# Optimization experiments

Hardware: AMD Instinct MI355X
Metric: run time of the kernel (lower is better)

Reference implementation:

```python
import jax, jax.numpy as jnp
import numpy as np

B, S, D = 4, 1024, 384
NUM_ITEMS = 16384
NUM_CLUSTERS = 256
MAX_CLUSTER_SIZE = 128  # 16384/256 = 64 real members, padded to 128 with -1
NEG_INF = -1e9


def setup_inputs() -> dict:
    key = jax.random.key(0)
    k1, k2, k3, k4, k5 = jax.random.split(key, 5)
    hidden_states = jax.random.normal(k1, (B, S, D), dtype=jnp.float32)
    item_embeddings = jax.random.normal(k2, (NUM_ITEMS, D), dtype=jnp.float32) * 0.02
    cluster_embeddings = jax.random.normal(k3, (NUM_CLUSTERS, D), dtype=jnp.float32) * 0.02
    targets = jax.random.randint(k4, (B, S), 0, NUM_ITEMS, dtype=jnp.int32)
    item_mask = (jax.random.uniform(k5, (B, S)) < 0.8).astype(jnp.float32)
    # Deterministic round-robin clustering: item i -> cluster i % C, slot i // C
    cluster_assignments = (jnp.arange(NUM_ITEMS, dtype=jnp.int32) % NUM_CLUSTERS)
    ids = (jnp.arange(NUM_CLUSTERS, dtype=jnp.int32)[:, None]
           + NUM_CLUSTERS * jnp.arange(MAX_CLUSTER_SIZE, dtype=jnp.int32)[None, :])
    cluster_indices = jnp.where(ids < NUM_ITEMS, ids, -1)  # [C, M], padded with -1
    in_cluster_id = (jnp.arange(NUM_ITEMS, dtype=jnp.int32) // NUM_CLUSTERS)
    return {
        "hidden_states": hidden_states,
        "item_embeddings": item_embeddings,
        "cluster_embeddings": cluster_embeddings,
        "item_mask": item_mask,
        "targets": targets,
        "cluster_assignments": cluster_assignments,
        "cluster_indices": cluster_indices,
        "in_cluster_id": in_cluster_id,
    }


def reference(hidden_states, item_embeddings, cluster_embeddings, item_mask,
              targets, cluster_assignments, cluster_indices, in_cluster_id):
    # Level 1: cluster logits / log-probs
    cluster_logits = jnp.einsum('bsd,cd->bsc', hidden_states, cluster_embeddings)
    cluster_log_probs = jax.nn.log_softmax(cluster_logits, axis=-1)
    target_cluster_ids = cluster_assignments[targets]                      # [B,S]
    target_cluster_log_prob = jnp.take_along_axis(
        cluster_log_probs, target_cluster_ids[..., None].astype(jnp.int32), axis=-1
    ).squeeze(-1)                                                          # [B,S]

    # Level 2: gather member embeddings of the target cluster, masked softmax
    cluster_members = cluster_indices[target_cluster_ids]                  # [B,S,M]
    member_emb = item_embeddings[jnp.maximum(cluster_members, 0)]          # [B,S,M,D]
    member_logits = jnp.einsum('bsd,bsmd->bsm', hidden_states, member_emb)  # [B,S,M]
    masked_logits = jnp.where(cluster_members != -1, member_logits, NEG_INF)
    member_log_probs = jax.nn.log_softmax(masked_logits, axis=-1)
    target_pos = in_cluster_id[targets]                                    # [B,S]
    target_item_log_prob = jnp.take_along_axis(
        member_log_probs, target_pos[..., None].astype(jnp.int32), axis=-1
    ).squeeze(-1)

    # Combined loss
    loss_per_token = -(target_cluster_log_prob + target_item_log_prob)
    total_loss = jnp.sum(loss_per_token * item_mask) / (jnp.sum(item_mask) + 1e-8)

    cluster_preds = jnp.argmax(cluster_logits, axis=-1)
    cluster_acc = jnp.mean((cluster_preds == target_cluster_ids).astype(jnp.float32))

    dummy_logits = jnp.zeros(hidden_states.shape[:2] + (item_embeddings.shape[0],),
                             dtype=hidden_states.dtype)
    return (dummy_logits, total_loss,
            -jnp.mean(target_cluster_log_prob),
            -jnp.mean(target_item_log_prob),
            cluster_acc)
```

## Files before the change

kernel.cpp:

```cpp
#include <hip/hip_runtime.h>
#include <math.h>

#define Ddim 384
#define D4 96
#define NUM_ITEMS 16384
#define NUM_CLUSTERS 256
#define MCS 128
#define NEG_INF_F (-1e9f)
#define NTOK 4096
#define TPB 8
#define NCB (NTOK / TPB)
#define NFILLB 2048

__device__ __forceinline__ float dot4(const float4& a, const float4& b) {
    return a.x * b.x + a.y * b.y + a.z * b.z + a.w * b.w;
}

__global__ __launch_bounds__(256) void hs_fill_meta(
    const int* __restrict__ targets, const int* __restrict__ cluster_assign,
    float* __restrict__ dummy_out, int* __restrict__ wsI)
{
    const int tid = threadIdx.x;

    if (blockIdx.x == NFILLB) {
        __shared__ int cnt[NUM_CLUSTERS], scan[NUM_CLUSTERS], cur[NUM_CLUSTERS];
        cnt[tid] = 0; cur[tid] = 0;
        __syncthreads();
        int tcv[NTOK / 256];
        #pragma unroll
        for (int i = 0; i < NTOK / 256; ++i) {
            const int t = i * 256 + tid;
            const int tc = cluster_assign[targets[t]];
            tcv[i] = tc;
            atomicAdd(&cnt[tc], 1);
        }
        __syncthreads();
        scan[tid] = cnt[tid];
        __syncthreads();
        for (int d = 1; d < 256; d <<= 1) {
            const int v = (tid >= d) ? scan[tid - d] : 0;
            __syncthreads();
            scan[tid] += v;
            __syncthreads();
        }
        wsI[tid] = scan[tid] - cnt[tid];
        if (tid == 255) wsI[256] = NTOK;
        __syncthreads();
        #pragma unroll
        for (int i = 0; i < NTOK / 256; ++i) {
            const int t = i * 256 + tid;
            const int tc = tcv[i];
            const int p = atomicAdd(&cur[tc], 1);
            wsI[257 + (scan[tc] - cnt[tc]) + p] = t;
        }
        return;
    }

    const size_t base = (size_t)blockIdx.x * 256 + tid;
    float4 z; z.x = z.y = z.z = z.w = 0.f;
    float4* o4 = reinterpret_cast<float4*>(dummy_out) + base;
    #pragma unroll 8
    for (int i = 0; i < 32; ++i)
        o4[(size_t)i * (NFILLB * 256)] = z;
}

__global__ __launch_bounds__(512, 2) void hs_compute(
    const float* __restrict__ hidden,
    const float* __restrict__ item_emb,
    const float* __restrict__ cluster_emb,
    const float* __restrict__ item_mask,
    const int*   __restrict__ targets,
    const int*   __restrict__ cluster_assign,
    const int*   __restrict__ cluster_idx,
    const int*   __restrict__ in_cluster_id,
    const int*   __restrict__ wsI,
    float* __restrict__ ws)
{
    const int cb   = blockIdx.x;
    const int tid  = threadIdx.x;
    const int t0   = cb * TPB;
    const int lane = tid & 63;
    const int wave = tid >> 6;
    const int wq   = wave & 1;
    const int wqt  = wave >> 1;
    const int q    = lane >> 4;
    const int r    = lane & 15;

    __shared__ float clog[TPB][NUM_CLUSTERS];
    __shared__ float mlog[TPB][64];

    const int* list = wsI + 257;

    const float4* h4 = reinterpret_cast<const float4*>(hidden);
    int tok[4];
    #pragma unroll
    for (int j = 0; j < 4; ++j) tok[j] = list[t0 + wq * 4 + j];
    float4 hf[4][6];
    #pragma unroll
    for (int j = 0; j < 4; ++j)
        #pragma unroll
        for (int i = 0; i < 6; ++i)
            hf[j][i] = h4[(size_t)tok[j] * D4 + i * 16 + r];

    const float4* ce4 = reinterpret_cast<const float4*>(cluster_emb);
    #pragma unroll 2
    for (int it = 0; it < 16; ++it) {
        const int c = wqt * 64 + it * 4 + q;
        float4 ce[6];
        #pragma unroll
        for (int i = 0; i < 6; ++i) ce[i] = ce4[(size_t)c * D4 + i * 16 + r];
        float a0 = 0.f, a1 = 0.f, a2 = 0.f, a3 = 0.f;
        #pragma unroll
        for (int i = 0; i < 6; ++i) {
            a0 += dot4(ce[i], hf[0][i]);
            a1 += dot4(ce[i], hf[1][i]);
            a2 += dot4(ce[i], hf[2][i]);
            a3 += dot4(ce[i], hf[3][i]);
        }
        const bool hi8 = (r & 8) != 0;
        float u  = hi8 ? a1 : a0;
        float uS = hi8 ? a0 : a1;
        u += __shfl_xor(uS, 8);
        float w  = hi8 ? a3 : a2;
        float wS = hi8 ? a2 : a3;
        w += __shfl_xor(wS, 8);
        const bool hi4 = (r & 4) != 0;
        float zv = hi4 ? w : u;
        float zS = hi4 ? u : w;
        zv += __shfl_xor(zS, 4);
        zv += __shfl_xor(zv, 2);
        zv += __shfl_xor(zv, 1);
        if ((r & 3) == 0) {
            const int m = (r >> 2) & 3;
            const int tokj = (m == 1) ? 2 : (m == 2) ? 1 : m;
            clog[wq * 4 + tokj][c] = zv;
        }
    }
    __syncthreads();

    const int r8 = lane & 7;
    const int g8 = lane >> 3;
    const float4* ie4 = reinterpret_cast<const float4*>(item_emb);

    const int t  = wave;
    const int gt = list[t0 + t];
    const int tgt  = targets[gt];
    const int tc   = cluster_assign[tgt];
    const int tpos = in_cluster_id[tgt];
    const float msk = item_mask[gt];

    const float v0 = clog[t][lane];
    const float v1 = clog[t][lane + 64];
    const float v2 = clog[t][lane + 128];
    const float v3 = clog[t][lane + 192];
    float bv = v0; int bi = lane;
    if (v1 > bv) { bv = v1; bi = lane + 64;  }
    if (v2 > bv) { bv = v2; bi = lane + 128; }
    if (v3 > bv) { bv = v3; bi = lane + 192; }
    #pragma unroll
    for (int m = 32; m > 0; m >>= 1) {
        const float ov = __shfl_xor(bv, m);
        const int   oi = __shfl_xor(bi, m);
        if (ov > bv || (ov == bv && oi < bi)) { bv = ov; bi = oi; }
    }
    float e = expf(v0 - bv) + expf(v1 - bv) + expf(v2 - bv) + expf(v3 - bv);
    #pragma unroll
    for (int m = 32; m > 0; m >>= 1) e += __shfl_xor(e, m);
    const float lse = bv + logf(e);
    const float tlpc = clog[t][tc] - lse;

    float4 hme[12];
    #pragma unroll
    for (int i = 0; i < 12; ++i)
        hme[i] = h4[(size_t)gt * D4 + i * 8 + r8];
    const int* crow = cluster_idx + (size_t)tc * MCS;
    #pragma unroll 2
    for (int it = 0; it < 8; ++it) {
        const int id = crow[it * 8 + g8];
        const float4* ir = ie4 + (size_t)id * D4;
        float pa = 0.f;
        #pragma unroll
        for (int i = 0; i < 12; ++i) pa += dot4(ir[i * 8 + r8], hme[i]);
        pa += __shfl_xor(pa, 1);
        pa += __shfl_xor(pa, 2);
        pa += __shfl_xor(pa, 4);
        if (r8 == 0) mlog[t][it * 8 + g8] = pa;
    }
    const float w0 = mlog[t][lane];
    float mx = w0;
    #pragma unroll
    for (int m = 32; m > 0; m >>= 1) mx = fmaxf(mx, __shfl_xor(mx, m));
    float e2 = expf(w0 - mx);
    #pragma unroll
    for (int m = 32; m > 0; m >>= 1) e2 += __shfl_xor(e2, m);
    const float tlpi = mlog[t][tpos] - (mx + logf(e2));

    if (lane == 0) {
        ws[NTOK + gt]     = msk;
        ws[2 * NTOK + gt] = tlpc;
        ws[3 * NTOK + gt] = tlpi;
        ws[4 * NTOK + gt] = (bi == tc) ? 1.f : 0.f;
    }
}

__global__ __launch_bounds__(1024) void hs_final(
    const float* __restrict__ ws, float* __restrict__ out)
{
    __shared__ double red[5][1024];
    const int tid = threadIdx.x;
    double a0 = 0, a1 = 0, a2 = 0, a3 = 0, a4 = 0;
    for (int i = tid; i < NTOK; i += 1024) {
        const float msk  = ws[NTOK + i];
        const float tlpc = ws[2 * NTOK + i];
        const float tlpi = ws[3 * NTOK + i];
        a0 += (double)(-(tlpc + tlpi) * msk);
        a1 += (double)msk;
        a2 += (double)tlpc;
        a3 += (double)tlpi;
        a4 += (double)ws[4 * NTOK + i];
    }
    red[0][tid] = a0; red[1][tid] = a1; red[2][tid] = a2;
    red[3][tid] = a3; red[4][tid] = a4;
    __syncthreads();
    for (int s2 = 512; s2 > 0; s2 >>= 1) {
        if (tid < s2) {
            red[0][tid] += red[0][tid + s2];
            red[1][tid] += red[1][tid + s2];
            red[2][tid] += red[2][tid + s2];
            red[3][tid] += red[3][tid + s2];
            red[4][tid] += red[4][tid + s2];
        }
        __syncthreads();
    }
    if (tid == 0) {
        out[0] = (float)(red[0][0] / (red[1][0] + 1e-8));
        out[1] = (float)(-red[2][0] / (double)NTOK);
        out[2] = (float)(-red[3][0] / (double)NTOK);
        out[3] = (float)(red[4][0] / (double)NTOK);
    }
}

extern "C" void kernel_launch(void* const* d_in, const int* in_sizes, int n_in,
                              void* d_out, int out_size, void* d_ws, size_t ws_size,
                              hipStream_t stream) {
    const float* hidden         = (const float*)d_in[0];
    const float* item_emb       = (const float*)d_in[1];
    const float* cluster_emb    = (const float*)d_in[2];
    const float* item_mask      = (const float*)d_in[3];
    const int*   targets        = (const int*)d_in[4];
    const int*   cluster_assign = (const int*)d_in[5];
    const int*   cluster_idx    = (const int*)d_in[6];
    const int*   in_cluster_id  = (const int*)d_in[7];

    float* out = (float*)d_out;
    float* ws  = (float*)d_ws;
    int*   wsI = (int*)(ws + 5 * NTOK);

    const size_t dummy_elems = (size_t)NTOK * NUM_ITEMS;

    hs_fill_meta<<<NFILLB + 1, 256, 0, stream>>>(
        targets, cluster_assign, out, wsI);
    hs_compute<<<NCB, 512, 0, stream>>>(
        hidden, item_emb, cluster_emb, item_mask, targets,
        cluster_assign, cluster_idx, in_cluster_id, wsI, ws);
    hs_final<<<1, 1024, 0, stream>>>(ws, out + dummy_elems);
}
```

Measured before the change: 108.2 us.

## Use 256-thread blocks with each wave scoring all eight tokens per cluster

The compute kernel drops to 4 waves per block. Each wave now holds hidden-state fragments for all 8 tokens and scores 64 clusters against them, so every cluster row is loaded once per block instead of twice. The shuffle reduction is reworked to a 5-bit lane split, and an empty asm pins the hidden registers. Each wave then runs the member-softmax phase for 2 tokens in turn, which reduces parallelism in that phase and raises register pressure.

```diff
diff --git a/kernel.cpp b/kernel.cpp
--- a/kernel.cpp
+++ b/kernel.cpp
@@ -15,6 +15,9 @@
 __device__ __forceinline__ float dot4(const float4& a, const float4& b) {
     return a.x * b.x + a.y * b.y + a.z * b.z + a.w * b.w;
 }
+__device__ __forceinline__ void pin4(float4& v) {
+    asm volatile("" : "+v"(v.x), "+v"(v.y), "+v"(v.z), "+v"(v.w));
+}
 
 __global__ __launch_bounds__(256) void hs_fill_meta(
     const int* __restrict__ targets, const int* __restrict__ cluster_assign,
@@ -64,7 +67,7 @@
         o4[(size_t)i * (NFILLB * 256)] = z;
 }
 
-__global__ __launch_bounds__(512, 2) void hs_compute(
+__global__ __launch_bounds__(256, 2) void hs_compute(
     const float* __restrict__ hidden,
     const float* __restrict__ item_emb,
     const float* __restrict__ cluster_emb,
@@ -81,10 +84,8 @@
     const int t0   = cb * TPB;
     const int lane = tid & 63;
     const int wave = tid >> 6;
-    const int wq   = wave & 1;
-    const int wqt  = wave >> 1;
-    const int q    = lane >> 4;
-    const int r    = lane & 15;
+    const int q2   = lane >> 5;
+    const int r5   = lane & 31;
 
     __shared__ float clog[TPB][NUM_CLUSTERS];
     __shared__ float mlog[TPB][64];
@@ -92,48 +93,60 @@
     const int* list = wsI + 257;
 
     const float4* h4 = reinterpret_cast<const float4*>(hidden);
-    int tok[4];
+    int tok[8];
     #pragma unroll
-    for (int j = 0; j < 4; ++j) tok[j] = list[t0 + wq * 4 + j];
-    float4 hf[4][6];
+    for (int j = 0; j < 8; ++j) tok[j] = list[t0 + j];
+    float4 hf[8][3];
     #pragma unroll
-    for (int j = 0; j < 4; ++j)
-        #pragma unroll
-        for (int i = 0; i < 6; ++i)
-            hf[j][i] = h4[(size_t)tok[j] * D4 + i * 16 + r];
+    for (int j = 0; j < 8; ++j)
+        #pragma unroll
+        for (int i = 0; i < 3; ++i) {
+            hf[j][i] = h4[(size_t)tok[j] * D4 + i * 32 + r5];
+            pin4(hf[j][i]);
+        }
 
     const float4* ce4 = reinterpret_cast<const float4*>(cluster_emb);
     #pragma unroll 2
-    for (int it = 0; it < 16; ++it) {
-        const int c = wqt * 64 + it * 4 + q;
-        float4 ce[6];
-        #pragma unroll
-        for (int i = 0; i < 6; ++i) ce[i] = ce4[(size_t)c * D4 + i * 16 + r];
+    for (int it = 0; it < 32; ++it) {
+        const int c = wave * 64 + it * 2 + q2;
+        float4 ce[3];
+        #pragma unroll
+        for (int i = 0; i < 3; ++i) ce[i] = ce4[(size_t)c * D4 + i * 32 + r5];
         float a0 = 0.f, a1 = 0.f, a2 = 0.f, a3 = 0.f;
-        #pragma unroll
-        for (int i = 0; i < 6; ++i) {
+        float a4 = 0.f, a5 = 0.f, a6 = 0.f, a7 = 0.f;
+        #pragma unroll
+        for (int i = 0; i < 3; ++i) {
             a0 += dot4(ce[i], hf[0][i]);
             a1 += dot4(ce[i], hf[1][i]);
             a2 += dot4(ce[i], hf[2][i]);
             a3 += dot4(ce[i], hf[3][i]);
-        }
-        const bool hi8 = (r & 8) != 0;
-        float u  = hi8 ? a1 : a0;
-        float uS = hi8 ? a0 : a1;
-        u += __shfl_xor(uS, 8);
-        float w  = hi8 ? a3 : a2;
-        float wS = hi8 ? a2 : a3;
-        w += __shfl_xor(wS, 8);
-        const bool hi4 = (r & 4) != 0;
-        float zv = hi4 ? w : u;
-        float zS = hi4 ? u : w;
-        zv += __shfl_xor(zS, 4);
-        zv += __shfl_xor(zv, 2);
-        zv += __shfl_xor(zv, 1);
-        if ((r & 3) == 0) {
-            const int m = (r >> 2) & 3;
-            const int tokj = (m == 1) ? 2 : (m == 2) ? 1 : m;
-            clog[wq * 4 + tokj][c] = zv;
+            a4 += dot4(ce[i], hf[4][i]);
+            a5 += dot4(ce[i], hf[5][i]);
+            a6 += dot4(ce[i], hf[6][i]);
+            a7 += dot4(ce[i], hf[7][i]);
+        }
+        const bool h16 = (r5 & 16) != 0;
+        float u0 = h16 ? a4 : a0, uS0 = h16 ? a0 : a4;
+        float u1 = h16 ? a5 : a1, uS1 = h16 ? a1 : a5;
+        float u2 = h16 ? a6 : a2, uS2 = h16 ? a2 : a6;
+        float u3 = h16 ? a7 : a3, uS3 = h16 ? a3 : a7;
+        u0 += __shfl_xor(uS0, 16);
+        u1 += __shfl_xor(uS1, 16);
+        u2 += __shfl_xor(uS2, 16);
+        u3 += __shfl_xor(uS3, 16);
+        const bool h8 = (r5 & 8) != 0;
+        float v0 = h8 ? u2 : u0, vS0 = h8 ? u0 : u2;
+        float v1 = h8 ? u3 : u1, vS1 = h8 ? u1 : u3;
+        v0 += __shfl_xor(vS0, 8);
+        v1 += __shfl_xor(vS1, 8);
+        const bool h4b = (r5 & 4) != 0;
+        float w = h4b ? v1 : v0, wS = h4b ? v0 : v1;
+        w += __shfl_xor(wS, 4);
+        w += __shfl_xor(w, 2);
+        w += __shfl_xor(w, 1);
+        if ((r5 & 3) == 0) {
+            const int T = ((r5 >> 4) & 1) * 4 + ((r5 >> 3) & 1) * 2 + ((r5 >> 2) & 1);
+            clog[T][c] = w;
         }
     }
     __syncthreads();
@@ -142,64 +155,67 @@
     const int g8 = lane >> 3;
     const float4* ie4 = reinterpret_cast<const float4*>(item_emb);
 
-    const int t  = wave;
-    const int gt = list[t0 + t];
-    const int tgt  = targets[gt];
-    const int tc   = cluster_assign[tgt];
-    const int tpos = in_cluster_id[tgt];
-    const float msk = item_mask[gt];
-
-    const float v0 = clog[t][lane];
-    const float v1 = clog[t][lane + 64];
-    const float v2 = clog[t][lane + 128];
-    const float v3 = clog[t][lane + 192];
-    float bv = v0; int bi = lane;
-    if (v1 > bv) { bv = v1; bi = lane + 64;  }
-    if (v2 > bv) { bv = v2; bi = lane + 128; }
-    if (v3 > bv) { bv = v3; bi = lane + 192; }
     #pragma unroll
-    for (int m = 32; m > 0; m >>= 1) {
-        const float ov = __shfl_xor(bv, m);
-        const int   oi = __shfl_xor(bi, m);
-        if (ov > bv || (ov == bv && oi < bi)) { bv = ov; bi = oi; }
-    }
-    float e = expf(v0 - bv) + expf(v1 - bv) + expf(v2 - bv) + expf(v3 - bv);
-    #pragma unroll
-    for (int m = 32; m > 0; m >>= 1) e += __shfl_xor(e, m);
-    const float lse = bv + logf(e);
-    const float tlpc = clog[t][tc] - lse;
-
-    float4 hme[12];
-    #pragma unroll
-    for (int i = 0; i < 12; ++i)
-        hme[i] = h4[(size_t)gt * D4 + i * 8 + r8];
-    const int* crow = cluster_idx + (size_t)tc * MCS;
-    #pragma unroll 2
-    for (int it = 0; it < 8; ++it) {
-        const int id = crow[it * 8 + g8];
-        const float4* ir = ie4 + (size_t)id * D4;
-        float pa = 0.f;
-        #pragma unroll
-        for (int i = 0; i < 12; ++i) pa += dot4(ir[i * 8 + r8], hme[i]);
-        pa += __shfl_xor(pa, 1);
-        pa += __shfl_xor(pa, 2);
-        pa += __shfl_xor(pa, 4);
-        if (r8 == 0) mlog[t][it * 8 + g8] = pa;
-    }
-    const float w0 = mlog[t][lane];
-    float mx = w0;
-    #pragma unroll
-    for (int m = 32; m > 0; m >>= 1) mx = fmaxf(mx, __shfl_xor(mx, m));
-    float e2 = expf(w0 - mx);
-    #pragma unroll
-    for (int m = 32; m > 0; m >>= 1) e2 += __shfl_xor(e2, m);
-    const float tlpi = mlog[t][tpos] - (mx + logf(e2));
-
-    if (lane == 0) {
-        ws[NTOK + gt]     = msk;
-        ws[2 * NTOK + gt] = tlpc;
-        ws[3 * NTOK + gt] = tlpi;
-        ws[4 * NTOK + gt] = (bi == tc) ? 1.f : 0.f;
+    for (int p = 0; p < 2; ++p) {
+        const int t  = wave * 2 + p;
+        const int gt = list[t0 + t];
+        const int tgt  = targets[gt];
+        const int tc   = cluster_assign[tgt];
+        const int tpos = in_cluster_id[tgt];
+        const float msk = item_mask[gt];
+
+        const float v0 = clog[t][lane];
+        const float v1 = clog[t][lane + 64];
+        const float v2 = clog[t][lane + 128];
+        const float v3 = clog[t][lane + 192];
+        float bv = v0; int bi = lane;
+        if (v1 > bv) { bv = v1; bi = lane + 64;  }
+        if (v2 > bv) { bv = v2; bi = lane + 128; }
+        if (v3 > bv) { bv = v3; bi = lane + 192; }
+        #pragma unroll
+        for (int m = 32; m > 0; m >>= 1) {
+            const float ov = __shfl_xor(bv, m);
+            const int   oi = __shfl_xor(bi, m);
+            if (ov > bv || (ov == bv && oi < bi)) { bv = ov; bi = oi; }
+        }
+        float e = expf(v0 - bv) + expf(v1 - bv) + expf(v2 - bv) + expf(v3 - bv);
+        #pragma unroll
+        for (int m = 32; m > 0; m >>= 1) e += __shfl_xor(e, m);
+        const float lse = bv + logf(e);
+        const float tlpc = clog[t][tc] - lse;
+
+        float4 hme[12];
+        #pragma unroll
+        for (int i = 0; i < 12; ++i)
+            hme[i] = h4[(size_t)gt * D4 + i * 8 + r8];
+        const int* crow = cluster_idx + (size_t)tc * MCS;
+        #pragma unroll 2
+        for (int it = 0; it < 8; ++it) {
+            const int id = crow[it * 8 + g8];
+            const float4* ir = ie4 + (size_t)id * D4;
+            float pa = 0.f;
+            #pragma unroll
+            for (int i = 0; i < 12; ++i) pa += dot4(ir[i * 8 + r8], hme[i]);
+            pa += __shfl_xor(pa, 1);
+            pa += __shfl_xor(pa, 2);
+            pa += __shfl_xor(pa, 4);
+            if (r8 == 0) mlog[t][it * 8 + g8] = pa;
+        }
+        const float w0 = mlog[t][lane];
+        float mx = w0;
+        #pragma unroll
+        for (int m = 32; m > 0; m >>= 1) mx = fmaxf(mx, __shfl_xor(mx, m));
+        float e2 = expf(w0 - mx);
+        #pragma unroll
+        for (int m = 32; m > 0; m >>= 1) e2 += __shfl_xor(e2, m);
+        const float tlpi = mlog[t][tpos] - (mx + logf(e2));
+
+        if (lane == 0) {
+            ws[NTOK + gt]     = msk;
+            ws[2 * NTOK + gt] = tlpc;
+            ws[3 * NTOK + gt] = tlpi;
+            ws[4 * NTOK + gt] = (bi == tc) ? 1.f : 0.f;
+        }
     }
 }
 
@@ -260,7 +276,7 @@
 
     hs_fill_meta<<<NFILLB + 1, 256, 0, stream>>>(
         targets, cluster_assign, out, wsI);
-    hs_compute<<<NCB, 512, 0, stream>>>(
+    hs_compute<<<NCB, 256, 0, stream>>>(
         hidden, item_emb, cluster_emb, item_mask, targets,
         cluster_assign, cluster_idx, in_cluster_id, wsI, ws);
     hs_final<<<1, 1024, 0, stream>>>(ws, out + dummy_elems);
```

Result: slower. 120.8 us (+11.7%).
